# Optimization experiments

Hardware: AMD Instinct MI355X
Metric: run time of the kernel (lower is better)

## Reference

```python
import jax, jax.numpy as jnp
import numpy as np

TEMPERATURE = 0.07
EPS = 1e-8  # torch cosine_similarity clamps the norm product at eps


def setup_inputs() -> dict:
    key = jax.random.key(0)
    k1, k2 = jax.random.split(key)
    B, D = 8192, 256
    u = jax.random.normal(k1, (B, D), dtype=jnp.float32)
    v = jax.random.normal(k2, (B, D), dtype=jnp.float32)
    return {"u": u, "v": v}


def _cos_sim_matrix(a, b):
    # pairwise cosine similarity: (a . b) / max(|a||b|, eps)
    dots = a @ b.T                                   # [B, B]
    an = jnp.linalg.norm(a, axis=-1)                 # [B]
    bn = jnp.linalg.norm(b, axis=-1)                 # [B]
    denom = jnp.maximum(an[:, None] * bn[None, :], EPS)
    return dots / denom


def reference(u, v):
    B = u.shape[0]
    sim_uv = _cos_sim_matrix(u, v) / TEMPERATURE     # [B, B]
    sim_uu = _cos_sim_matrix(u, u) / TEMPERATURE     # [B, B]
    eye = jnp.eye(B, dtype=bool)
    pos_loss = jnp.diagonal(sim_uv)                  # [B]
    neg_inf = jnp.array(-jnp.inf, dtype=sim_uv.dtype)
    # off-diagonal entries of both matrices, concatenated per row (2B-2 valid each)
    negative_sim = jnp.concatenate(
        [jnp.where(eye, neg_inf, sim_uv), jnp.where(eye, neg_inf, sim_uu)], axis=1
    )                                                # [B, 2B]
    neg_loss = jax.nn.logsumexp(negative_sim, axis=-1)  # [B]
    return (-pos_loss + neg_loss).mean()
```

## Files before the change

### kernel.cpp

```cpp
#include <hip/hip_runtime.h>
#include <hip/hip_bf16.h>
#include <stdint.h>

#define NB 8192
#define ND 256
#define NW 16384
#define BM 128
#define BN 64
#define NSTRIP 4
#define STRIPW 4096
#define NTILES (STRIPW / BN)
#define NU (NTILES * 2)
#define SQRT_INVT 3.7796447f

typedef __bf16 bf16x8 __attribute__((ext_vector_type(8)));
typedef float floatx4 __attribute__((ext_vector_type(4)));

__device__ __forceinline__ void gload_lds16(const void* g, void* l) {
    __builtin_amdgcn_global_load_lds(
        (const __attribute__((address_space(1))) unsigned int*)g,
        (__attribute__((address_space(3))) unsigned int*)l,
        16, 0, 0);
}

__global__ __launch_bounds__(512) void prep_kernel(
    const float* __restrict__ u, const float* __restrict__ v,
    __hip_bfloat16* __restrict__ W, float* __restrict__ out)
{
    const int t    = threadIdx.x;
    if (blockIdx.x == 0 && t == 0) out[0] = 0.f;
    const int row  = blockIdx.x * 8 + (t >> 6);
    const int lane = t & 63;
    const float* src = (row < NB) ? (v + (size_t)row * ND)
                                  : (u + (size_t)(row - NB) * ND);
    float4 x = ((const float4*)src)[lane];
    float ss = x.x * x.x + x.y * x.y + x.z * x.z + x.w * x.w;
#pragma unroll
    for (int off = 1; off < 64; off <<= 1) ss += __shfl_xor(ss, off, 64);
    const float sc = rsqrtf(ss) * SQRT_INVT;
    ushort4 o;
    __hip_bfloat16 h;
    h = __float2bfloat16(x.x * sc); o.x = *(const unsigned short*)&h;
    h = __float2bfloat16(x.y * sc); o.y = *(const unsigned short*)&h;
    h = __float2bfloat16(x.z * sc); o.z = *(const unsigned short*)&h;
    h = __float2bfloat16(x.w * sc); o.w = *(const unsigned short*)&h;
    ((ushort4*)(W + (size_t)row * ND))[lane] = o;
}

__global__ __launch_bounds__(512, 2) void dcl_main(
    const __hip_bfloat16* __restrict__ W,
    float* __restrict__ partial,
    float* __restrict__ pos)
{
    const int b  = blockIdx.x;
    const int s  = (b >> 1) & 3;
    const int rt = ((b >> 3) << 1) | (b & 1);
    const int rb = rt * BM;

    const __hip_bfloat16* A = W + (size_t)NB * ND;

    __shared__ __align__(16) char lds[131072];

    const int tid  = threadIdx.x;
    const int wave = tid >> 6;
    const int lane = tid & 63;
    const int wm   = wave >> 2;
    const int wn   = wave & 3;
    const int quad = lane >> 4;
    const int tcol = lane & 15;
    const int rh4  = lane >> 4;
    const int cc   = lane & 15;

    char* const wbuf  = lds + wave * 16384;
    const int   sbase = s * STRIPW;

#define STAGE(u) do {                                                        \
    const int tu_ = (u) >> 1, h_ = (u) & 1;                                  \
    const int rowb_ = sbase + tu_ * BN + wn * 16;                            \
    char* dst_ = wbuf + ((u) & 3) * 4096;                                    \
    _Pragma("unroll")                                                        \
    for (int i_ = 0; i_ < 4; i_++) {                                         \
        int r_ = i_ * 4 + rh4;                                               \
        gload_lds16(W + (size_t)(rowb_ + r_) * ND + h_ * 128                 \
                      + ((cc ^ r_) << 3),                                    \
                    dst_ + i_ * 1024);                                       \
    }                                                                        \
} while (0)

#define COMPUTE_HALF(u) do {                                                 \
    const char* sb_ = wbuf + ((u) & 3) * 4096;                               \
    const int h_ = (u) & 1;                                                  \
    __builtin_amdgcn_s_setprio(1);                                           \
    _Pragma("unroll")                                                        \
    for (int ks_ = 0; ks_ < 4; ks_++) {                                      \
        bf16x8 bb_ = *(const bf16x8*)(sb_ + tcol * 256 +                     \
                                      ((((ks_ * 4) + quad) ^ tcol) << 4));   \
        _Pragma("unroll")                                                    \
        for (int mt_ = 0; mt_ < 4; mt_++)                                    \
            acc[mt_] = __builtin_amdgcn_mfma_f32_16x16x32_bf16(              \
                af[mt_][h_ * 4 + ks_], bb_, acc[mt_], 0, 0, 0);              \
    }                                                                        \
    __builtin_amdgcn_s_setprio(0);                                           \
} while (0)

#define ACC_INIT() do {                                                      \
    _Pragma("unroll")                                                        \
    for (int mt_ = 0; mt_ < 4; mt_++) acc[mt_] = (floatx4){0.f,0.f,0.f,0.f}; \
} while (0)

#define WAITV(n) do {                                                        \
    asm volatile("s_waitcnt vmcnt(" #n ")" ::: "memory");                    \
    __builtin_amdgcn_sched_barrier(0);                                       \
} while (0)

#define EPILOGUE(t) do {                                                     \
    const int cb_ = sbase + (t) * BN;                                        \
    if (cb_ != dp) {                                                         \
        _Pragma("unroll")                                                    \
        for (int mt_ = 0; mt_ < 4; mt_++)                                    \
            _Pragma("unroll")                                                \
            for (int rg_ = 0; rg_ < 4; rg_++)                                \
                rsum[mt_][rg_] += __expf(acc[mt_][rg_]);                     \
    } else {                                                                 \
        _Pragma("unroll")                                                    \
        for (int mt_ = 0; mt_ < 4; mt_++)                                    \
            _Pragma("unroll")                                                \
            for (int rg_ = 0; rg_ < 4; rg_++) {                              \
                int rl_ = mt_ * 16 + quad * 4 + rg_;                         \
                bool sel_ = (rl_ == wn * 16 + tcol);                         \
                float sc_ = acc[mt_][rg_];                                   \
                if (isuv && sel_) pos[rb + wm * 64 + rl_] = sc_;             \
                rsum[mt_][rg_] += sel_ ? 0.f : __expf(sc_);                  \
            }                                                                \
    }                                                                        \
} while (0)

    STAGE(0); STAGE(1); STAGE(2);

    bf16x8 af[4][8];
#pragma unroll
    for (int mt = 0; mt < 4; mt++) {
        const __hip_bfloat16* ar =
            A + (size_t)(rb + wm * 64 + mt * 16 + tcol) * ND + quad * 8;
#pragma unroll
        for (int ks = 0; ks < 8; ks++)
            af[mt][ks] = *(const bf16x8*)(ar + ks * 32);
    }

    const bool isuv = (s < 2);
    int dp = rb + wm * 64 + (isuv ? 0 : NB);
    if ((dp >> 12) != s) dp = 0x40000000;

    float rsum[4][4];
#pragma unroll
    for (int mt = 0; mt < 4; mt++)
#pragma unroll
        for (int rg = 0; rg < 4; rg++) rsum[mt][rg] = 0.f;

    floatx4 acc[4];

#pragma unroll 1
    for (int t = 0; t < NTILES - 2; t++) {
        const int u0 = 2 * t;
        ACC_INIT();
        STAGE(u0 + 3);
        WAITV(12);
        COMPUTE_HALF(u0);
        STAGE(u0 + 4);
        WAITV(12);
        COMPUTE_HALF(u0 + 1);
        __builtin_amdgcn_sched_barrier(0);
        EPILOGUE(t);
    }
    {
        ACC_INIT();
        STAGE(127);
        WAITV(12); COMPUTE_HALF(124);
        WAITV(8);  COMPUTE_HALF(125);
        __builtin_amdgcn_sched_barrier(0);
        EPILOGUE(62);
    }
    {
        ACC_INIT();
        WAITV(4);  COMPUTE_HALF(126);
        WAITV(0);  COMPUTE_HALF(127);
        __builtin_amdgcn_sched_barrier(0);
        EPILOGUE(63);
    }

#undef STAGE
#undef COMPUTE_HALF
#undef ACC_INIT
#undef WAITV
#undef EPILOGUE

    __syncthreads();

#pragma unroll
    for (int mt = 0; mt < 4; mt++)
#pragma unroll
        for (int reg = 0; reg < 4; reg++) {
            float vsum = rsum[mt][reg];
            vsum += __shfl_xor(vsum, 1, 64);
            vsum += __shfl_xor(vsum, 2, 64);
            vsum += __shfl_xor(vsum, 4, 64);
            vsum += __shfl_xor(vsum, 8, 64);
            if (tcol == 0) {
                int lrow = wm * 64 + mt * 16 + quad * 4 + reg;
                ((float*)lds)[wn * 128 + lrow] = vsum;
            }
        }
    __syncthreads();
    if (tid < BM) {
        const float* lf = (const float*)lds;
        float t = lf[tid] + lf[128 + tid] + lf[256 + tid] + lf[384 + tid];
        partial[(size_t)s * NB + rb + tid] = t;
    }
}

__global__ __launch_bounds__(256) void finalize_kernel(
    const float* __restrict__ partial, const float* __restrict__ pos,
    float* __restrict__ out)
{
    const int i = blockIdx.x * 256 + threadIdx.x;
    float tot = partial[i] + partial[NB + i] + partial[2 * NB + i]
              + partial[3 * NB + i];
    float sv = logf(tot) - pos[i];
#pragma unroll
    for (int off = 32; off > 0; off >>= 1) sv += __shfl_down(sv, off, 64);
    __shared__ float wsum[4];
    const int t = threadIdx.x;
    if ((t & 63) == 0) wsum[t >> 6] = sv;
    __syncthreads();
    if (t == 0) {
        float blk = (wsum[0] + wsum[1]) + (wsum[2] + wsum[3]);
        atomicAdd(out, blk / (float)NB);
    }
}

extern "C" void kernel_launch(void* const* d_in, const int* in_sizes, int n_in,
                              void* d_out, int out_size, void* d_ws, size_t ws_size,
                              hipStream_t stream) {
    const float* u = (const float*)d_in[0];
    const float* v = (const float*)d_in[1];
    float* out = (float*)d_out;

    char* ws = (char*)d_ws;
    __hip_bfloat16* W = (__hip_bfloat16*)ws;
    float* partial = (float*)(ws + (size_t)NW * ND * sizeof(__hip_bfloat16));
    float* pos     = partial + NSTRIP * NB;

    prep_kernel<<<NW / 8, 512, 0, stream>>>(u, v, W, out);
    dcl_main<<<256, 512, 0, stream>>>(W, partial, pos);
    finalize_kernel<<<NB / 256, 256, 0, stream>>>(partial, pos, out);
}
```

Before: 144.7 us.

## Share B-panel staging across waves and software-pipeline epilogue with double accumulators

```diff
diff --git a/kernel.cpp b/kernel.cpp
--- a/kernel.cpp
+++ b/kernel.cpp
@@ -9,8 +9,7 @@
 #define BN 64
 #define NSTRIP 4
 #define STRIPW 4096
-#define NTILES (STRIPW / BN)
-#define NU (NTILES * 2)
+#define NPANEL (STRIPW / BN)
 #define SQRT_INVT 3.7796447f
 
 typedef __bf16 bf16x8 __attribute__((ext_vector_type(8)));
@@ -68,59 +67,48 @@
     const int wn   = wave & 3;
     const int quad = lane >> 4;
     const int tcol = lane & 15;
-    const int rh4  = lane >> 4;
-    const int cc   = lane & 15;
-
-    char* const wbuf  = lds + wave * 16384;
-    const int   sbase = s * STRIPW;
-
-#define STAGE(u) do {                                                        \
-    const int tu_ = (u) >> 1, h_ = (u) & 1;                                  \
-    const int rowb_ = sbase + tu_ * BN + wn * 16;                            \
-    char* dst_ = wbuf + ((u) & 3) * 4096;                                    \
+
+    const int sbase = s * STRIPW;
+
+#define WAITV(N) asm volatile("s_waitcnt vmcnt(" #N ")" ::: "memory")
+
+#define STAGE(T, SLOT) do {                                                  \
+    const int cbS_ = sbase + (T) * BN;                                       \
+    char* dstS_ = lds + (SLOT) * 32768;                                      \
     _Pragma("unroll")                                                        \
     for (int i_ = 0; i_ < 4; i_++) {                                         \
-        int r_ = i_ * 4 + rh4;                                               \
-        gload_lds16(W + (size_t)(rowb_ + r_) * ND + h_ * 128                 \
-                      + ((cc ^ r_) << 3),                                    \
-                    dst_ + i_ * 1024);                                       \
+        int o_ = i_ * 8192 + wave * 1024 + lane * 16;                        \
+        int r_ = o_ >> 9;                                 \
+        int c_ = (o_ >> 4) & 31;                              \
+        int cg_ = (c_ ^ (r_ & 15)) * 8;               \
+        gload_lds16(W + (size_t)(cbS_ + r_) * ND + cg_,                      \
+                    dstS_ + i_ * 8192 + wave * 1024);                        \
     }                                                                        \
 } while (0)
 
-#define COMPUTE_HALF(u) do {                                                 \
-    const char* sb_ = wbuf + ((u) & 3) * 4096;                               \
-    const int h_ = (u) & 1;                                                  \
-    __builtin_amdgcn_s_setprio(1);                                           \
+#define COMPUTE(SLOT, ACC) do {                                              \
+    const char* sbC_ = lds + (SLOT) * 32768;                                 \
     _Pragma("unroll")                                                        \
-    for (int ks_ = 0; ks_ < 4; ks_++) {                                      \
-        bf16x8 bb_ = *(const bf16x8*)(sb_ + tcol * 256 +                     \
+    for (int mt_ = 0; mt_ < 4; mt_++) ACC[mt_] = (floatx4){0.f,0.f,0.f,0.f}; \
+    _Pragma("unroll")                                                        \
+    for (int ks_ = 0; ks_ < 8; ks_++) {                                      \
+        bf16x8 bb_ = *(const bf16x8*)(sbC_ + (wn * 16 + tcol) * 512 +        \
                                       ((((ks_ * 4) + quad) ^ tcol) << 4));   \
         _Pragma("unroll")                                                    \
         for (int mt_ = 0; mt_ < 4; mt_++)                                    \
-            acc[mt_] = __builtin_amdgcn_mfma_f32_16x16x32_bf16(              \
-                af[mt_][h_ * 4 + ks_], bb_, acc[mt_], 0, 0, 0);              \
+            ACC[mt_] = __builtin_amdgcn_mfma_f32_16x16x32_bf16(              \
+                af[mt_][ks_], bb_, ACC[mt_], 0, 0, 0);                       \
     }                                                                        \
-    __builtin_amdgcn_s_setprio(0);                                           \
-} while (0)
-
-#define ACC_INIT() do {                                                      \
-    _Pragma("unroll")                                                        \
-    for (int mt_ = 0; mt_ < 4; mt_++) acc[mt_] = (floatx4){0.f,0.f,0.f,0.f}; \
-} while (0)
-
-#define WAITV(n) do {                                                        \
-    asm volatile("s_waitcnt vmcnt(" #n ")" ::: "memory");                    \
-    __builtin_amdgcn_sched_barrier(0);                                       \
-} while (0)
-
-#define EPILOGUE(t) do {                                                     \
-    const int cb_ = sbase + (t) * BN;                                        \
-    if (cb_ != dp) {                                                         \
+} while (0)
+
+#define EPIFIX(ACCP, TP) do {                                                \
+    const int cbP_ = sbase + (TP) * BN;                                      \
+    if (cbP_ != dp) {                                                        \
         _Pragma("unroll")                                                    \
         for (int mt_ = 0; mt_ < 4; mt_++)                                    \
             _Pragma("unroll")                                                \
             for (int rg_ = 0; rg_ < 4; rg_++)                                \
-                rsum[mt_][rg_] += __expf(acc[mt_][rg_]);                     \
+                rsum[mt_][rg_] += __expf(ACCP[mt_][rg_]);                    \
     } else {                                                                 \
         _Pragma("unroll")                                                    \
         for (int mt_ = 0; mt_ < 4; mt_++)                                    \
@@ -128,14 +116,22 @@
             for (int rg_ = 0; rg_ < 4; rg_++) {                              \
                 int rl_ = mt_ * 16 + quad * 4 + rg_;                         \
                 bool sel_ = (rl_ == wn * 16 + tcol);                         \
-                float sc_ = acc[mt_][rg_];                                   \
-                if (isuv && sel_) pos[rb + wm * 64 + rl_] = sc_;             \
+                float sc_ = ACCP[mt_][rg_];                                  \
+                if (sel_) posv = sc_;                                        \
                 rsum[mt_][rg_] += sel_ ? 0.f : __expf(sc_);                  \
             }                                                                \
     }                                                                        \
 } while (0)
 
-    STAGE(0); STAGE(1); STAGE(2);
+#define PANEL(T, SLOT, ACCC, ACCP, NW, DOSTAGE) do {                         \
+    WAITV(NW);                                                               \
+    __builtin_amdgcn_s_barrier();                                            \
+    if (DOSTAGE) STAGE((T) + 3, ((SLOT) + 3) & 3);                           \
+    __builtin_amdgcn_s_setprio(1);                                           \
+    COMPUTE(SLOT, ACCC);                                                     \
+    EPIFIX(ACCP, (T) - 1);                                                   \
+    __builtin_amdgcn_s_setprio(0);                                           \
+} while (0)
 
     bf16x8 af[4][8];
 #pragma unroll
@@ -147,9 +143,12 @@
             af[mt][ks] = *(const bf16x8*)(ar + ks * 32);
     }
 
+    STAGE(0, 0); STAGE(1, 1); STAGE(2, 2);
+
     const bool isuv = (s < 2);
     int dp = rb + wm * 64 + (isuv ? 0 : NB);
-    if ((dp >> 12) != s) dp = 0x40000000;
+    const bool dvalid = ((dp >> 12) == s);
+    if (!dvalid) dp = 0x40000000;
 
     float rsum[4][4];
 #pragma unroll
@@ -157,42 +156,33 @@
 #pragma unroll
         for (int rg = 0; rg < 4; rg++) rsum[mt][rg] = 0.f;
 
-    floatx4 acc[4];
+    float posv = 0.f;
+    floatx4 accA[4], accB[4];
+#pragma unroll
+    for (int mt = 0; mt < 4; mt++)
+        accB[mt] = (floatx4){-1e38f, -1e38f, -1e38f, -1e38f};
 
 #pragma unroll 1
-    for (int t = 0; t < NTILES - 2; t++) {
-        const int u0 = 2 * t;
-        ACC_INIT();
-        STAGE(u0 + 3);
-        WAITV(12);
-        COMPUTE_HALF(u0);
-        STAGE(u0 + 4);
-        WAITV(12);
-        COMPUTE_HALF(u0 + 1);
-        __builtin_amdgcn_sched_barrier(0);
-        EPILOGUE(t);
-    }
-    {
-        ACC_INIT();
-        STAGE(127);
-        WAITV(12); COMPUTE_HALF(124);
-        WAITV(8);  COMPUTE_HALF(125);
-        __builtin_amdgcn_sched_barrier(0);
-        EPILOGUE(62);
-    }
-    {
-        ACC_INIT();
-        WAITV(4);  COMPUTE_HALF(126);
-        WAITV(0);  COMPUTE_HALF(127);
-        __builtin_amdgcn_sched_barrier(0);
-        EPILOGUE(63);
-    }
-
+    for (int t = 0; t < NPANEL - 4; t += 4) {
+        PANEL(t + 0, 0, accA, accB, 8, 1);
+        PANEL(t + 1, 1, accB, accA, 8, 1);
+        PANEL(t + 2, 2, accA, accB, 8, 1);
+        PANEL(t + 3, 3, accB, accA, 8, 1);
+    }
+    PANEL(60, 0, accA, accB, 8, 1);
+    PANEL(61, 1, accB, accA, 8, 0);
+    PANEL(62, 2, accA, accB, 4, 0);
+    PANEL(63, 3, accB, accA, 0, 0);
+    EPIFIX(accB, 63);
+
+#undef WAITV
 #undef STAGE
-#undef COMPUTE_HALF
-#undef ACC_INIT
-#undef WAITV
-#undef EPILOGUE
+#undef COMPUTE
+#undef EPIFIX
+#undef PANEL
+
+    if (isuv && dvalid && (tcol >> 2) == quad)
+        pos[rb + wm * 64 + wn * 16 + tcol] = posv;
 
     __syncthreads();
 
```

Measured after the change: 285.5 us. 97.3% more time.

## Split column strips into eight shards, shrink LDS ring, use exp2 scaling

Applied to the files above, without the earlier changes.

```diff
diff --git a/kernel.cpp b/kernel.cpp
--- a/kernel.cpp
+++ b/kernel.cpp
@@ -7,11 +7,11 @@
 #define NW 16384
 #define BM 128
 #define BN 64
-#define NSTRIP 4
-#define STRIPW 4096
-#define NTILES (STRIPW / BN)
-#define NU (NTILES * 2)
-#define SQRT_INVT 3.7796447f
+#define NSH 8
+#define SHW 2048
+#define NPANEL_B (SHW / BN)
+#define SQRT_SCALE 4.53981596f
+#define LN2F 0.69314718f
 
 typedef __bf16 bf16x8 __attribute__((ext_vector_type(8)));
 typedef float floatx4 __attribute__((ext_vector_type(4)));
@@ -37,7 +37,7 @@
     float ss = x.x * x.x + x.y * x.y + x.z * x.z + x.w * x.w;
 #pragma unroll
     for (int off = 1; off < 64; off <<= 1) ss += __shfl_xor(ss, off, 64);
-    const float sc = rsqrtf(ss) * SQRT_INVT;
+    const float sc = rsqrtf(ss) * SQRT_SCALE;
     ushort4 o;
     __hip_bfloat16 h;
     h = __float2bfloat16(x.x * sc); o.x = *(const unsigned short*)&h;
@@ -53,13 +53,15 @@
     float* __restrict__ pos)
 {
     const int b  = blockIdx.x;
-    const int s  = (b >> 1) & 3;
-    const int rt = ((b >> 3) << 1) | (b & 1);
+    const int x  = b & 7;
+    const int j  = b >> 3;
+    const int sh = ((x & 3) << 1) | (j & 1);
+    const int rt = (j >> 1) | ((x >> 2) << 5);
     const int rb = rt * BM;
 
     const __hip_bfloat16* A = W + (size_t)NB * ND;
 
-    __shared__ __align__(16) char lds[131072];
+    __shared__ __align__(16) char lds[65536];
 
     const int tid  = threadIdx.x;
     const int wave = tid >> 6;
@@ -71,13 +73,18 @@
     const int rh4  = lane >> 4;
     const int cc   = lane & 15;
 
-    char* const wbuf  = lds + wave * 16384;
-    const int   sbase = s * STRIPW;
+    char* const wbuf  = lds + wave * 8192;
+    const int   sbase = sh * SHW;
+
+#define WAITV(N) do {                                                        \
+    asm volatile("s_waitcnt vmcnt(" #N ")" ::: "memory");                    \
+    __builtin_amdgcn_sched_barrier(0);                                       \
+} while (0)
 
 #define STAGE(u) do {                                                        \
     const int tu_ = (u) >> 1, h_ = (u) & 1;                                  \
     const int rowb_ = sbase + tu_ * BN + wn * 16;                            \
-    char* dst_ = wbuf + ((u) & 3) * 4096;                                    \
+    char* dst_ = wbuf + ((u) & 1) * 4096;                                    \
     _Pragma("unroll")                                                        \
     for (int i_ = 0; i_ < 4; i_++) {                                         \
         int r_ = i_ * 4 + rh4;                                               \
@@ -88,7 +95,7 @@
 } while (0)
 
 #define COMPUTE_HALF(u) do {                                                 \
-    const char* sb_ = wbuf + ((u) & 3) * 4096;                               \
+    const char* sb_ = wbuf + ((u) & 1) * 4096;                               \
     const int h_ = (u) & 1;                                                  \
     __builtin_amdgcn_s_setprio(1);                                           \
     _Pragma("unroll")                                                        \
@@ -108,19 +115,14 @@
     for (int mt_ = 0; mt_ < 4; mt_++) acc[mt_] = (floatx4){0.f,0.f,0.f,0.f}; \
 } while (0)
 
-#define WAITV(n) do {                                                        \
-    asm volatile("s_waitcnt vmcnt(" #n ")" ::: "memory");                    \
-    __builtin_amdgcn_sched_barrier(0);                                       \
-} while (0)
-
-#define EPILOGUE(t) do {                                                     \
-    const int cb_ = sbase + (t) * BN;                                        \
+#define EPILOGUE(p) do {                                                     \
+    const int cb_ = sbase + (p) * BN;                                        \
     if (cb_ != dp) {                                                         \
         _Pragma("unroll")                                                    \
         for (int mt_ = 0; mt_ < 4; mt_++)                                    \
             _Pragma("unroll")                                                \
             for (int rg_ = 0; rg_ < 4; rg_++)                                \
-                rsum[mt_][rg_] += __expf(acc[mt_][rg_]);                     \
+                rsum[mt_][rg_] += exp2f(acc[mt_][rg_]);                      \
     } else {                                                                 \
         _Pragma("unroll")                                                    \
         for (int mt_ = 0; mt_ < 4; mt_++)                                    \
@@ -129,13 +131,11 @@
                 int rl_ = mt_ * 16 + quad * 4 + rg_;                         \
                 bool sel_ = (rl_ == wn * 16 + tcol);                         \
                 float sc_ = acc[mt_][rg_];                                   \
-                if (isuv && sel_) pos[rb + wm * 64 + rl_] = sc_;             \
-                rsum[mt_][rg_] += sel_ ? 0.f : __expf(sc_);                  \
+                if (sel_) posv = sc_;                                        \
+                rsum[mt_][rg_] += sel_ ? 0.f : exp2f(sc_);                   \
             }                                                                \
     }                                                                        \
 } while (0)
-
-    STAGE(0); STAGE(1); STAGE(2);
 
     bf16x8 af[4][8];
 #pragma unroll
@@ -147,9 +147,12 @@
             af[mt][ks] = *(const bf16x8*)(ar + ks * 32);
     }
 
-    const bool isuv = (s < 2);
+    STAGE(0); STAGE(1);
+
+    const bool isuv = (sh < 4);
     int dp = rb + wm * 64 + (isuv ? 0 : NB);
-    if ((dp >> 12) != s) dp = 0x40000000;
+    const bool dvalid = ((dp >> 11) == sh);
+    if (!dvalid) dp = 0x40000000;
 
     float rsum[4][4];
 #pragma unroll
@@ -157,42 +160,38 @@
 #pragma unroll
         for (int rg = 0; rg < 4; rg++) rsum[mt][rg] = 0.f;
 
+    float posv = 0.f;
     floatx4 acc[4];
 
 #pragma unroll 1
-    for (int t = 0; t < NTILES - 2; t++) {
-        const int u0 = 2 * t;
+    for (int p = 0; p < NPANEL_B - 1; p++) {
+        const int u0 = 2 * p;
         ACC_INIT();
+        WAITV(4);
+        COMPUTE_HALF(u0);
+        STAGE(u0 + 2);
+        WAITV(4);
+        COMPUTE_HALF(u0 + 1);
         STAGE(u0 + 3);
-        WAITV(12);
-        COMPUTE_HALF(u0);
-        STAGE(u0 + 4);
-        WAITV(12);
-        COMPUTE_HALF(u0 + 1);
         __builtin_amdgcn_sched_barrier(0);
-        EPILOGUE(t);
+        EPILOGUE(p);
     }
     {
         ACC_INIT();
-        STAGE(127);
-        WAITV(12); COMPUTE_HALF(124);
-        WAITV(8);  COMPUTE_HALF(125);
+        WAITV(4);  COMPUTE_HALF(62);
+        WAITV(0);  COMPUTE_HALF(63);
         __builtin_amdgcn_sched_barrier(0);
-        EPILOGUE(62);
-    }
-    {
-        ACC_INIT();
-        WAITV(4);  COMPUTE_HALF(126);
-        WAITV(0);  COMPUTE_HALF(127);
-        __builtin_amdgcn_sched_barrier(0);
-        EPILOGUE(63);
-    }
-
+        EPILOGUE(31);
+    }
+
+#undef WAITV
 #undef STAGE
 #undef COMPUTE_HALF
 #undef ACC_INIT
-#undef WAITV
 #undef EPILOGUE
+
+    if (isuv && dvalid && (tcol >> 2) == quad)
+        pos[rb + wm * 64 + wn * 16 + tcol] = posv * LN2F;
 
     __syncthreads();
 
@@ -214,7 +213,7 @@
     if (tid < BM) {
         const float* lf = (const float*)lds;
         float t = lf[tid] + lf[128 + tid] + lf[256 + tid] + lf[384 + tid];
-        partial[(size_t)s * NB + rb + tid] = t;
+        partial[(size_t)sh * NB + rb + tid] = t;
     }
 }
 
@@ -223,8 +222,9 @@
     float* __restrict__ out)
 {
     const int i = blockIdx.x * 256 + threadIdx.x;
-    float tot = partial[i] + partial[NB + i] + partial[2 * NB + i]
-              + partial[3 * NB + i];
+    float tot = 0.f;
+#pragma unroll
+    for (int k = 0; k < NSH; k++) tot += partial[(size_t)k * NB + i];
     float sv = logf(tot) - pos[i];
 #pragma unroll
     for (int off = 32; off > 0; off >>= 1) sv += __shfl_down(sv, off, 64);
@@ -248,9 +248,9 @@
     char* ws = (char*)d_ws;
     __hip_bfloat16* W = (__hip_bfloat16*)ws;
     float* partial = (float*)(ws + (size_t)NW * ND * sizeof(__hip_bfloat16));
-    float* pos     = partial + NSTRIP * NB;
+    float* pos     = partial + NSH * NB;
 
     prep_kernel<<<NW / 8, 512, 0, stream>>>(u, v, W, out);
-    dcl_main<<<256, 512, 0, stream>>>(W, partial, pos);
+    dcl_main<<<512, 512, 0, stream>>>(W, partial, pos);
     finalize_kernel<<<NB / 256, 256, 0, stream>>>(partial, pos, out);
 }
```

New measurement: 155.8 us. 1.08x slower.
